# Kernel tuning notes

Measured on AMD Instinct MI355X. Metric: run time of the kernel, lower is better.

The kernel has to match this reference:

```python
import jax, jax.numpy as jnp
import numpy as np

C = 64  # chunk size, fixed in the original module


def setup_inputs() -> dict:
    key = jax.random.key(0)
    k1, k2, k3, k4, k5 = jax.random.split(key, 5)
    B, T, D, H = 4, 4096, 1024, 8
    out = jax.random.normal(k1, (B, T, D), jnp.float32)
    W_write = jax.random.normal(k2, (D, D), jnp.float32) * 0.02
    # original inits proj_read to zeros; use small random weight so the memory path is exercised
    W_read = jax.random.normal(k3, (D, D), jnp.float32) * 0.02
    W_beta = jax.random.normal(k4, (H, D), jnp.float32) * 0.02
    decay = 4.6 + jax.random.normal(k5, (H,), jnp.float32) * 0.1
    return {"out": out, "W_write": W_write, "W_read": W_read, "W_beta": W_beta, "decay": decay}


def reference(out, W_write, W_read, W_beta, decay):
    B, T, D = out.shape
    H = decay.shape[0]
    d = D // H
    assert T % C == 0  # chosen shapes avoid padding (pad_len == 0 path)
    N = T // C

    x = out.astype(jnp.float32)
    xh = x.reshape(B, T, H, d)
    rk = xh / jnp.maximum(jnp.linalg.norm(xh, axis=-1, keepdims=True), 1e-12)
    rk = rk.transpose(0, 2, 1, 3)                                   # (B,H,T,d) read keys
    wk = jnp.pad(rk[:, :, :-1], ((0, 0), (0, 0), (1, 0), (0, 0)))    # write keys = shifted read keys
    v = (x @ W_write.T).reshape(B, T, H, d).transpose(0, 2, 1, 3)    # (B,H,T,d)
    beta = jax.nn.sigmoid(x @ W_beta.T).transpose(0, 2, 1)[..., None]  # (B,H,T,1)
    v = v * beta
    wk_beta = wk * beta

    log_gamma = jnp.log(jax.nn.sigmoid(decay))                       # (H,)
    pos = jnp.arange(C, dtype=jnp.float32)
    cum_decay = (pos + 1.0) * log_gamma[:, None]                     # (H,C)
    tril = jnp.tril(jnp.ones((C, C), jnp.float32))
    L_mask = jnp.exp((cum_decay[:, :, None] - cum_decay[:, None, :]) * tril) * tril  # (H,C,C)
    decay_exp = jnp.exp(cum_decay)[:, :, None]                       # (H,C,1)
    chunk_total = jnp.exp(cum_decay[:, -1])[:, None, None]           # (H,1,1)
    dw = jnp.exp(cum_decay[:, -1:] - cum_decay)[:, :, None]          # (H,C,1)

    rk_c = rk.reshape(B, H, N, C, d)
    wk_c = wk.reshape(B, H, N, C, d)
    v_c = v.reshape(B, H, N, C, d)
    wkb_c = wk_beta.reshape(B, H, N, C, d)

    # UT transform: A = strictly-lower part of -(beta K)(K^T) with decay, then forward substitution
    strict_lower = jnp.tril(jnp.ones((C, C), bool), -1)
    A = -(wkb_c @ jnp.swapaxes(wk_c, -1, -2)) * L_mask[None, :, None]
    A = jnp.where(strict_lower, A, 0.0)

    def ut_body(i, A):
        row = A[..., i, :]                                           # (B,H,N,C)
        new_row = row + jnp.einsum('bhnj,bhnjk->bhnk', row, A)
        return A.at[..., i, :].set(new_row)

    A = jax.lax.fori_loop(1, C, ut_body, A)
    A = A + jnp.eye(C, dtype=A.dtype)

    v_c = A @ v_c
    wk_cum = A @ (wkb_c * decay_exp[None, :, None])

    # cross-chunk state recurrence
    causal = jnp.tril(jnp.ones((C, C), bool))                        # keep diag + lower
    xs = (jnp.moveaxis(rk_c, 2, 0), jnp.moveaxis(wk_c, 2, 0),
          jnp.moveaxis(v_c, 2, 0), jnp.moveaxis(wk_cum, 2, 0))
    S0 = jnp.zeros((B, H, d, d), jnp.float32)

    def chunk_step(S, xs_i):
        rk_i, wk_i, v_i, wkc_i = xs_i                                # each (B,H,C,d)
        attn = (rk_i @ jnp.swapaxes(wk_i, -1, -2)) * L_mask[None]
        attn = jnp.where(causal, attn, 0.0)
        v_new = v_i - wkc_i @ S
        o_i = (rk_i * decay_exp[None]) @ S + attn @ v_new
        S_new = chunk_total[None] * S + jnp.swapaxes(wk_i * dw[None], -1, -2) @ v_new
        return S_new, o_i

    _, o = jax.lax.scan(chunk_step, S0, xs)                          # (N,B,H,C,d)
    o = jnp.moveaxis(o, 0, 2).reshape(B, H, T, d).transpose(0, 2, 1, 3).reshape(B, T, D)
    return out + (o @ W_read.T).astype(out.dtype)
```

## Files before the change

kernel.cpp:

```cpp
#include <hip/hip_runtime.h>
#include <hip/hip_bf16.h>
#include <math.h>


#define T_LEN 4096
typedef unsigned short ushort;
typedef __attribute__((ext_vector_type(2))) unsigned short us2;
typedef __attribute__((ext_vector_type(4))) unsigned short us4;
typedef __attribute__((ext_vector_type(8))) unsigned short us8;
typedef __attribute__((ext_vector_type(8))) short short8v;
typedef __attribute__((ext_vector_type(4))) float f32x4;

__device__ __forceinline__ float bf2f(ushort u) {
  union { unsigned int u; float f; } c; c.u = ((unsigned int)u) << 16; return c.f;
}
__device__ __forceinline__ ushort f2bf(float x) {
  union { float f; unsigned int u; } c; c.f = x;
  unsigned int u = c.u + 0x7FFFu + ((c.u >> 16) & 1u);
  return (ushort)(u >> 16);
}

__global__ __launch_bounds__(256) void k_wcvt(
    const float* __restrict__ Ww, const float* __restrict__ Wr,
    ushort* __restrict__ Wwb, ushort* __restrict__ Wrb)
{
  size_t i = ((size_t)blockIdx.x * 256 + threadIdx.x) * 8;
  float4 p0 = *(const float4*)(Ww + i), p1 = *(const float4*)(Ww + i + 4);
  us8 o;
  o[0]=f2bf(p0.x); o[1]=f2bf(p0.y); o[2]=f2bf(p0.z); o[3]=f2bf(p0.w);
  o[4]=f2bf(p1.x); o[5]=f2bf(p1.y); o[6]=f2bf(p1.z); o[7]=f2bf(p1.w);
  *(us8*)(Wwb + i) = o;
  float4 q0 = *(const float4*)(Wr + i), q1 = *(const float4*)(Wr + i + 4);
  us8 o2;
  o2[0]=f2bf(q0.x); o2[1]=f2bf(q0.y); o2[2]=f2bf(q0.z); o2[3]=f2bf(q0.w);
  o2[4]=f2bf(q1.x); o2[5]=f2bf(q1.y); o2[6]=f2bf(q1.z); o2[7]=f2bf(q1.w);
  *(us8*)(Wrb + i) = o2;
}

__global__ __launch_bounds__(128) void k_prep(
    const float* __restrict__ x, const float* __restrict__ Wb,
    ushort* __restrict__ rk, float* __restrict__ beta, ushort* __restrict__ xb)
{
  int bt = blockIdx.x;
  int b = bt >> 12, t = bt & 4095;
  int tid = threadIdx.x;
  __shared__ float xs[1024];
  __shared__ float red[16];
  {
    const float4* x4 = (const float4*)(x + (size_t)bt * 1024);
    float4* xs4 = (float4*)xs;
    xs4[tid] = x4[tid];
    xs4[tid + 128] = x4[tid + 128];
  }
  __syncthreads();
  int h = tid >> 4;
  int e0 = h * 128 + (tid & 15) * 8;
  float ss = 0.f;
  #pragma unroll
  for (int s = 0; s < 8; ++s) { float v = xs[e0 + s]; ss += v * v; }
  #pragma unroll
  for (int m = 1; m < 16; m <<= 1) ss += __shfl_xor(ss, m, 64);
  float inv = 1.f / fmaxf(sqrtf(ss), 1e-12f);
  {
    int bh = b * 8 + h;
    us8 o;
    #pragma unroll
    for (int s = 0; s < 8; ++s) o[s] = f2bf(xs[e0 + s] * inv);
    *(us8*)(rk + ((size_t)bh * T_LEN + t) * 128 + (tid & 15) * 8) = o;
  }
  {
    us8 o;
    #pragma unroll
    for (int s = 0; s < 8; ++s) o[s] = f2bf(xs[tid * 8 + s]);
    *(us8*)(xb + (size_t)bt * 1024 + tid * 8) = o;
  }
  const float* xk = xs + tid * 8;
  #pragma unroll
  for (int h2 = 0; h2 < 8; ++h2) {
    const float* wb = Wb + (size_t)h2 * 1024 + tid * 8;
    float p = 0.f;
    #pragma unroll
    for (int s = 0; s < 8; ++s) p += xk[s] * wb[s];
    #pragma unroll
    for (int m = 1; m < 64; m <<= 1) p += __shfl_xor(p, m, 64);
    if ((tid & 63) == 0) red[(tid >> 6) * 8 + h2] = p;
  }
  __syncthreads();
  if (tid < 8) {
    float s = red[tid] + red[8 + tid];
    beta[((size_t)(b * 8 + tid)) * T_LEN + t] = 1.f / (1.f + expf(-s));
  }
}

#define LDK 40
template<int MODE>
__global__ __launch_bounds__(256) void k_gemm(
    const ushort* __restrict__ A, const ushort* __restrict__ Wb,
    const float* __restrict__ beta, const float* __restrict__ xadd,
    void* __restrict__ out_)
{
  __shared__ ushort As[128 * LDK];
  __shared__ ushort Bs[128 * LDK];
  const int n0 = blockIdx.x * 128;
  const int m0 = blockIdx.y * 128;
  const int tid = threadIdx.x;
  const int lane = tid & 63;
  const int wid = tid >> 6;
  const int wr = wid >> 1, wc = wid & 1;
  const int c = lane & 15, g = lane >> 4;
  const int srow = tid >> 2;
  const int seg = tid & 3;

  f32x4 acc[4][4] = {};

  for (int k0 = 0; k0 < 1024; k0 += 32) {
    {
      us8 o0 = *(const us8*)(A + (size_t)(m0 + srow) * 1024 + k0 + seg * 8);
      us8 o1 = *(const us8*)(A + (size_t)(m0 + srow + 64) * 1024 + k0 + seg * 8);
      *(us8*)&As[srow * LDK + seg * 8] = o0;
      *(us8*)&As[(srow + 64) * LDK + seg * 8] = o1;
    }
    {
      us8 o0 = *(const us8*)(Wb + (size_t)(n0 + srow) * 1024 + k0 + seg * 8);
      us8 o1 = *(const us8*)(Wb + (size_t)(n0 + srow + 64) * 1024 + k0 + seg * 8);
      *(us8*)&Bs[srow * LDK + seg * 8] = o0;
      *(us8*)&Bs[(srow + 64) * LDK + seg * 8] = o1;
    }
    __syncthreads();
    short8v af[4], bf[4];
    #pragma unroll
    for (int mi = 0; mi < 4; ++mi)
      af[mi] = *(const short8v*)&As[(wr * 64 + mi * 16 + c) * LDK + g * 8];
    #pragma unroll
    for (int ni = 0; ni < 4; ++ni)
      bf[ni] = *(const short8v*)&Bs[(wc * 64 + ni * 16 + c) * LDK + g * 8];
    #pragma unroll
    for (int mi = 0; mi < 4; ++mi)
      #pragma unroll
      for (int ni = 0; ni < 4; ++ni)
        acc[mi][ni] = __builtin_amdgcn_mfma_f32_16x16x32_bf16(af[mi], bf[ni], acc[mi][ni], 0, 0, 0);
    __syncthreads();
  }

  if (MODE == 0) {
    ushort* vb = (ushort*)out_;
    const int hh = n0 >> 7;
    #pragma unroll
    for (int mi = 0; mi < 4; ++mi) {
      #pragma unroll
      for (int ni = 0; ni < 4; ++ni) {
        int jc = wc * 64 + ni * 16 + c;
        #pragma unroll
        for (int j = 0; j < 4; ++j) {
          int m = m0 + wr * 64 + mi * 16 + g * 4 + j;
          int b = m >> 12, t = m & 4095;
          size_t base = (size_t)(b * 8 + hh) * T_LEN + t;
          float bv = beta[base];
          vb[base * 128 + jc] = f2bf(acc[mi][ni][j] * bv);
        }
      }
    }
  } else {
    float* out = (float*)out_;
    #pragma unroll
    for (int mi = 0; mi < 4; ++mi) {
      #pragma unroll
      for (int ni = 0; ni < 4; ++ni) {
        int n = n0 + wc * 64 + ni * 16 + c;
        #pragma unroll
        for (int j = 0; j < 4; ++j) {
          int m = m0 + wr * 64 + mi * 16 + g * 4 + j;
          size_t idx = (size_t)m * 1024 + n;
          out[idx] = xadd[idx] + acc[mi][ni][j];
        }
      }
    }
  }
}

__global__ __launch_bounds__(256) void k_chunk(
    const ushort* __restrict__ rk, ushort* __restrict__ vb,
    ushort* __restrict__ wkcum, ushort* __restrict__ attn,
    const float* __restrict__ beta, const float* __restrict__ decay,
    ushort* __restrict__ wkdwT)
{
  int bh = blockIdx.x >> 6;
  int n = blockIdx.x & 63;
  int h = bh & 7;
  int tid = threadIdx.x;
  int lane = tid & 63, w = tid >> 6;
  int c = lane & 15, g = lane >> 4;

  __shared__ __align__(16) char smem[39952];
  ushort* rkb  = (ushort*)smem;
  float*  redp = (float*)smem;
  ushort* Ab1  = (ushort*)smem;
  ushort* Ab2  = (ushort*)(smem + 9216);
  float*  Af   = (float*)(smem + 21760);
  ushort* xT   = (ushort*)(smem + 18432);
  float*  gpow  = (float*)(smem + 39168);
  float*  betaS = (float*)(smem + 39432);
  float*  bd    = (float*)(smem + 39688);

  float lg = logf(1.f / (1.f + expf(-decay[h])));
  if (tid < 65) gpow[tid] = expf(lg * (float)tid);
  if (tid < 64) betaS[tid] = beta[(size_t)bh * T_LEN + n * 64 + tid];
  const int t0 = n * 64;
  const size_t bhbase = (size_t)bh * T_LEN;
  const us8 zero8 = {0, 0, 0, 0, 0, 0, 0, 0};

  #pragma unroll
  for (int u = 0; u < 5; ++u) {
    int idx = tid + u * 256;
    int row = idx >> 4, cb = idx & 15;
    us8 v = zero8;
    int t = t0 + row - 1;
    if (row <= 64 && t >= 0) v = *(const us8*)(rk + (bhbase + t) * 128 + cb * 8);
    *(us8*)&rkb[row * 136 + cb * 8] = v;
  }
  for (int idx = tid; idx < 64 * 68; idx += 256) Af[idx] = 0.f;
  __syncthreads();
  if (tid < 64) bd[tid] = betaS[tid] * gpow[tid + 1];

  const size_t abase = ((size_t)bh * 64 + n) * 4096;
  {
    const int TR[14] = {0,1,1,2,2,2,3,3,3,3,4,4,4,4};
    const int TC[14] = {0,0,1,0,1,2,0,1,2,3,0,1,2,3};
    #pragma unroll
    for (int ti = 0; ti < 14; ++ti) {
      if ((ti & 3) != w) continue;
      const int tr = TR[ti], tc = TC[ti];
      f32x4 acc = {0.f, 0.f, 0.f, 0.f};
      #pragma unroll
      for (int ks = 0; ks < 4; ++ks) {
        short8v a = *(const short8v*)&rkb[(tr * 16 + c) * 136 + ks * 32 + g * 8];
        short8v b = *(const short8v*)&rkb[(tc * 16 + c) * 136 + ks * 32 + g * 8];
        acc = __builtin_amdgcn_mfma_f32_16x16x32_bf16(a, b, acc, 0, 0, 0);
      }
      #pragma unroll
      for (int r = 0; r < 4; ++r) {
        int a_ = tr * 16 + g * 4 + r;
        int j = tc * 16 + c;
        float val = acc[r];
        if (a_ <= 63) Af[a_ * 68 + j] = (a_ > j) ? (-betaS[a_] * val * gpow[a_ - j]) : 0.f;
        if (a_ >= 1 && a_ <= 64) {
          if (j <= a_ - 1)      attn[abase + (size_t)(a_ - 1) * 64 + j] = f2bf(val * gpow[a_ - 1 - j]);
          else if (a_ <= 63)    attn[abase + (size_t)(a_ - 1) * 64 + j] = 0;
        }
      }
    }
  }
  {
    const int ZR[6] = {0,0,0,1,1,2};
    const int ZC[6] = {1,2,3,2,3,3};
    int rr = tid >> 4, cc2 = tid & 15;
    #pragma unroll
    for (int z = 0; z < 6; ++z) {
      int r_att = ZR[z] * 16 - 1 + rr;
      if (r_att >= 0) attn[abase + (size_t)r_att * 64 + ZC[z] * 16 + cc2] = 0;
    }
  }
  __syncthreads();

  {
    int k = tid & 63, sp = tid >> 6;
    for (int i = 1; i < 64; ++i) {
      float part = 0.f;
      #pragma unroll
      for (int jj = 0; jj < 16; ++jj) {
        int j = sp * 16 + jj;
        part += Af[i * 68 + j] * Af[j * 68 + k];
      }
      redp[sp * 64 + k] = part;
      __syncthreads();
      if (tid < 64) Af[i * 68 + tid] += redp[tid] + redp[64 + tid] + redp[128 + tid] + redp[192 + tid];
      __syncthreads();
    }
  }
  {
    int i = tid >> 2, j0 = (tid & 3) * 16;
    #pragma unroll
    for (int jj = 0; jj < 16; ++jj) {
      int j = j0 + jj;
      float av = Af[i * 68 + j] + ((i == j) ? 1.f : 0.f);
      Ab1[i * 72 + j] = f2bf(av * bd[j]);
      Ab2[i * 72 + j] = f2bf(av);
    }
  }
  __syncthreads();

  #pragma unroll
  for (int u = 0; u < 4; ++u) {
    int idx = tid + u * 256;
    int j = idx & 63, eb = idx >> 6;
    int t = t0 + j - 1;
    us8 v = zero8;
    if (t >= 0) v = *(const us8*)(rk + (bhbase + t) * 128 + eb * 8);
    #pragma unroll
    for (int s = 0; s < 8; ++s) xT[(eb * 8 + s) * 72 + j] = v[s];
  }
  __syncthreads();

  {
    f32x4 acc[8] = {};
    #pragma unroll
    for (int ks = 0; ks < 2; ++ks) {
      short8v a = *(const short8v*)&Ab1[(w * 16 + c) * 72 + ks * 32 + g * 8];
      #pragma unroll
      for (int nt = 0; nt < 8; ++nt) {
        short8v b = *(const short8v*)&xT[(nt * 16 + c) * 72 + ks * 32 + g * 8];
        acc[nt] = __builtin_amdgcn_mfma_f32_16x16x32_bf16(a, b, acc[nt], 0, 0, 0);
      }
    }
    #pragma unroll
    for (int nt = 0; nt < 8; ++nt)
      #pragma unroll
      for (int r = 0; r < 4; ++r) {
        int i = w * 16 + g * 4 + r, e = nt * 16 + c;
        wkcum[(bhbase + t0 + i) * 128 + e] = f2bf(acc[nt][r]);
      }
  }
  {
    const size_t kbase = ((size_t)bh * 64 + n) * 8192;
    #pragma unroll
    for (int u = 0; u < 4; ++u) {
      int idx = tid + u * 256;
      int e = idx >> 3, seg = idx & 7;
      us8 v = *(const us8*)&xT[e * 72 + seg * 8];
      us8 o;
      #pragma unroll
      for (int s = 0; s < 8; ++s) o[s] = f2bf(bf2f(v[s]) * gpow[63 - (seg * 8 + s)]);
      *(us8*)(wkdwT + kbase + (size_t)e * 64 + seg * 8) = o;
    }
  }
  __syncthreads();
  #pragma unroll
  for (int u = 0; u < 4; ++u) {
    int idx = tid + u * 256;
    int j = idx & 63, eb = idx >> 6;
    us8 v = *(const us8*)(vb + (bhbase + t0 + j) * 128 + eb * 8);
    #pragma unroll
    for (int s = 0; s < 8; ++s) xT[(eb * 8 + s) * 72 + j] = v[s];
  }
  __syncthreads();
  {
    f32x4 acc[8] = {};
    #pragma unroll
    for (int ks = 0; ks < 2; ++ks) {
      short8v a = *(const short8v*)&Ab2[(w * 16 + c) * 72 + ks * 32 + g * 8];
      #pragma unroll
      for (int nt = 0; nt < 8; ++nt) {
        short8v b = *(const short8v*)&xT[(nt * 16 + c) * 72 + ks * 32 + g * 8];
        acc[nt] = __builtin_amdgcn_mfma_f32_16x16x32_bf16(a, b, acc[nt], 0, 0, 0);
      }
    }
    #pragma unroll
    for (int nt = 0; nt < 8; ++nt)
      #pragma unroll
      for (int r = 0; r < 4; ++r) {
        int i = w * 16 + g * 4 + r, e = nt * 16 + c;
        vb[(bhbase + t0 + i) * 128 + e] = f2bf(acc[nt][r]);
      }
  }
}

#define SCAN_STEP(W_, R_, T_, K_, V_, nW, nR, nT, nK, nV, n_) {                 \
  const int t0s = (n_) * 64;                                                    \
  { const int np = ((n_) < 63) ? (n_) + 1 : 63;                                 \
    const size_t rb = (bhbase + (size_t)(np * 64 + 16 * w + c)) * 128;          \
    _Pragma("unroll")                                                           \
    for (int ks = 0; ks < 4; ++ks) {                                            \
      nW[ks] = *(const short8v*)(wkcum + rb + ks * 32 + g * 8);                 \
      nR[ks] = *(const short8v*)(rk    + rb + ks * 32 + g * 8); }               \
    const size_t ab = ((size_t)bh * 64 + np) * 4096 + (size_t)(16 * w + c) * 64;\
    nT[0] = *(const short8v*)(attn + ab + g * 8);                               \
    nT[1] = *(const short8v*)(attn + ab + 32 + g * 8);                          \
    const size_t kb = ((size_t)bh * 64 + np) * 8192;                            \
    nK[0] = *(const short8v*)(wkdwT + kb + (size_t)(32 * w + c) * 64 + g * 8);  \
    nK[1] = *(const short8v*)(wkdwT + kb + (size_t)(32 * w + c) * 64 + 32 + g * 8); \
    nK[2] = *(const short8v*)(wkdwT + kb + (size_t)(32 * w + 16 + c) * 64 + g * 8); \
    nK[3] = *(const short8v*)(wkdwT + kb + (size_t)(32 * w + 16 + c) * 64 + 32 + g * 8); \
    _Pragma("unroll")                                                           \
    for (int r = 0; r < 4; ++r)                                                 \
      nV[r] = vb[(bhbase + (size_t)(np * 64 + 16 * w + 4 * g + r)) * 128 + q0 + c]; } \
  f32x4 accA = {}, accB = {};                                                   \
  _Pragma("unroll")                                                             \
  for (int ks = 0; ks < 4; ++ks) {                                              \
    short8v b0 = *(const short8v*)&ST[c * 136 + ks * 32 + g * 8];               \
    accA = __builtin_amdgcn_mfma_f32_16x16x32_bf16(W_[ks], b0, accA, 0, 0, 0);  \
    accB = __builtin_amdgcn_mfma_f32_16x16x32_bf16(R_[ks], b0, accB, 0, 0, 0); }\
  _Pragma("unroll")                                                             \
  for (int r = 0; r < 4; ++r) {                                                 \
    int i = 16 * w + 4 * g + r;                                                 \
    accB[r] *= gB[r];                                                           \
    vnL[c * 72 + i] = f2bf(bf2f(V_[r]) - accA[r]); }                            \
  asm volatile("s_waitcnt lgkmcnt(0)" ::: "memory");                            \
  __builtin_amdgcn_s_barrier();                                                 \
  short8v vf0 = *(const short8v*)&vnL[c * 72 + g * 8];                          \
  short8v vf1 = *(const short8v*)&vnL[c * 72 + 32 + g * 8];                     \
  accB = __builtin_amdgcn_mfma_f32_16x16x32_bf16(T_[0], vf0, accB, 0, 0, 0);    \
  accB = __builtin_amdgcn_mfma_f32_16x16x32_bf16(T_[1], vf1, accB, 0, 0, 0);    \
  _Pragma("unroll")                                                             \
  for (int r = 0; r < 4; ++r) {                                                 \
    int i = 16 * w + 4 * g + r;                                                 \
    og[((size_t)b_ * T_LEN + t0s + i) * 1024 + h * 128 + q0 + c] = f2bf(accB[r]); } \
  _Pragma("unroll")                                                             \
  for (int r = 0; r < 4; ++r) { accS0[r] *= ct; accS1[r] *= ct; }               \
  accS0 = __builtin_amdgcn_mfma_f32_16x16x32_bf16(K_[0], vf0, accS0, 0, 0, 0);  \
  accS0 = __builtin_amdgcn_mfma_f32_16x16x32_bf16(K_[1], vf1, accS0, 0, 0, 0);  \
  accS1 = __builtin_amdgcn_mfma_f32_16x16x32_bf16(K_[2], vf0, accS1, 0, 0, 0);  \
  accS1 = __builtin_amdgcn_mfma_f32_16x16x32_bf16(K_[3], vf1, accS1, 0, 0, 0);  \
  _Pragma("unroll")                                                             \
  for (int r = 0; r < 4; ++r) {                                                 \
    int p0r = 32 * w + 4 * g + r;                                               \
    ST[c * 136 + p0r]      = f2bf(accS0[r]);                                    \
    ST[c * 136 + p0r + 16] = f2bf(accS1[r]); }                                  \
  asm volatile("s_waitcnt lgkmcnt(0)" ::: "memory");                            \
  __builtin_amdgcn_s_barrier();                                                 \
}

__global__ __launch_bounds__(256) void k_scan_fused(
    const ushort* __restrict__ rk, const ushort* __restrict__ vb,
    const ushort* __restrict__ wkcum, const ushort* __restrict__ attn,
    const ushort* __restrict__ wkdwT, const float* __restrict__ decay,
    ushort* __restrict__ og)
{
  const int bh = blockIdx.x & 31;
  const int q0 = (blockIdx.x >> 5) * 16;
  const int b_ = bh >> 3, h = bh & 7;
  const int tid = threadIdx.x;
  const int lane = tid & 63, w = tid >> 6;
  const int c = lane & 15, g = lane >> 4;

  __shared__ ushort ST[16 * 136];
  __shared__ ushort vnL[16 * 72];
  __shared__ float gpow[65];

  float lg = logf(1.f / (1.f + expf(-decay[h])));
  if (tid < 65) gpow[tid] = expf(lg * (float)tid);
  for (int idx = tid; idx < 16 * 136; idx += 256) ST[idx] = 0;
  __syncthreads();
  const float ct = gpow[64];
  float gB[4];
  #pragma unroll
  for (int r = 0; r < 4; ++r) gB[r] = gpow[16 * w + 4 * g + r + 1];
  const size_t bhbase = (size_t)bh * T_LEN;

  f32x4 accS0 = {}, accS1 = {};
  short8v aW[4], aR[4], aT[2], aK[4];
  short8v bW[4], bR[4], bT[2], bK[4];
  ushort aV[4], bV[4];
  {
    const size_t rb = (bhbase + (size_t)(16 * w + c)) * 128;
    #pragma unroll
    for (int ks = 0; ks < 4; ++ks) {
      aW[ks] = *(const short8v*)(wkcum + rb + ks * 32 + g * 8);
      aR[ks] = *(const short8v*)(rk + rb + ks * 32 + g * 8);
    }
    const size_t ab = (size_t)bh * 64 * 4096 + (size_t)(16 * w + c) * 64;
    aT[0] = *(const short8v*)(attn + ab + g * 8);
    aT[1] = *(const short8v*)(attn + ab + 32 + g * 8);
    const size_t kb = (size_t)bh * 64 * 8192;
    aK[0] = *(const short8v*)(wkdwT + kb + (size_t)(32 * w + c) * 64 + g * 8);
    aK[1] = *(const short8v*)(wkdwT + kb + (size_t)(32 * w + c) * 64 + 32 + g * 8);
    aK[2] = *(const short8v*)(wkdwT + kb + (size_t)(32 * w + 16 + c) * 64 + g * 8);
    aK[3] = *(const short8v*)(wkdwT + kb + (size_t)(32 * w + 16 + c) * 64 + 32 + g * 8);
    #pragma unroll
    for (int r = 0; r < 4; ++r)
      aV[r] = vb[(bhbase + (size_t)(16 * w + 4 * g + r)) * 128 + q0 + c];
  }
  for (int n = 0; n < 64; n += 2) {
    SCAN_STEP(aW, aR, aT, aK, aV, bW, bR, bT, bK, bV, n);
    SCAN_STEP(bW, bR, bT, bK, bV, aW, aR, aT, aK, aV, n + 1);
  }
}

extern "C" void kernel_launch(void* const* d_in, const int* in_sizes, int n_in,
                              void* d_out, int out_size, void* d_ws, size_t ws_size,
                              hipStream_t stream) {
  const float* x   = (const float*)d_in[0];
  const float* Ww  = (const float*)d_in[1];
  const float* Wr  = (const float*)d_in[2];
  const float* Wb  = (const float*)d_in[3];
  const float* dec = (const float*)d_in[4];
  float* out = (float*)d_out;
  ushort* ws = (ushort*)d_ws;
  const size_t SZ = 16777216ull;
  ushort* rk    = ws;
  ushort* vb    = ws + SZ;
  ushort* wkcum = ws + 2 * SZ;
  ushort* og    = ws + 3 * SZ;
  ushort* attn  = ws + 4 * SZ;
  float*  beta  = (float*)(ws + 4 * SZ + 8388608ull);
  ushort* wkdwT = ws + 4 * SZ + 8388608ull + 262144ull;
  ushort* Wwb   = ws + 92536832ull;
  ushort* Wrb   = ws + 93585408ull;
  ushort* xb    = og;
  const size_t NEED = 189267968ull;
  if (ws_size < NEED) {
    hipMemcpyAsync(d_out, (const void*)x, (size_t)out_size * 4, hipMemcpyDeviceToDevice, stream);
    return;
  }

  k_wcvt<<<dim3(512), dim3(256), 0, stream>>>(Ww, Wr, Wwb, Wrb);
  k_prep<<<dim3(16384), dim3(128), 0, stream>>>(x, Wb, rk, beta, xb);
  k_gemm<0><<<dim3(8, 128), dim3(256), 0, stream>>>(xb, Wwb, beta, nullptr, (void*)vb);
  k_chunk<<<dim3(2048), dim3(256), 0, stream>>>(rk, vb, wkcum, attn, beta, dec, wkdwT);
  k_scan_fused<<<dim3(256), dim3(256), 0, stream>>>(rk, vb, wkcum, attn, wkdwT, dec, og);
  k_gemm<1><<<dim3(8, 128), dim3(256), 0, stream>>>(og, Wrb, nullptr, (const float*)x, (void*)out);
}
```

Measured before the change: 384.7 us.

## Run scan with a single wavefront per block to remove barriers

```diff
diff --git a/kernel.cpp b/kernel.cpp
--- a/kernel.cpp
+++ b/kernel.cpp
@@ -364,62 +364,103 @@
   }
 }
 
-#define SCAN_STEP(W_, R_, T_, K_, V_, nW, nR, nT, nK, nV, n_) {                 \
+#define SCAN1(CURW, CURV, NXTW, NXTV, n_) {                                     \
   const int t0s = (n_) * 64;                                                    \
+                                               \
   { const int np = ((n_) < 63) ? (n_) + 1 : 63;                                 \
-    const size_t rb = (bhbase + (size_t)(np * 64 + 16 * w + c)) * 128;          \
-    _Pragma("unroll")                                                           \
-    for (int ks = 0; ks < 4; ++ks) {                                            \
-      nW[ks] = *(const short8v*)(wkcum + rb + ks * 32 + g * 8);                 \
-      nR[ks] = *(const short8v*)(rk    + rb + ks * 32 + g * 8); }               \
-    const size_t ab = ((size_t)bh * 64 + np) * 4096 + (size_t)(16 * w + c) * 64;\
-    nT[0] = *(const short8v*)(attn + ab + g * 8);                               \
-    nT[1] = *(const short8v*)(attn + ab + 32 + g * 8);                          \
-    const size_t kb = ((size_t)bh * 64 + np) * 8192;                            \
-    nK[0] = *(const short8v*)(wkdwT + kb + (size_t)(32 * w + c) * 64 + g * 8);  \
-    nK[1] = *(const short8v*)(wkdwT + kb + (size_t)(32 * w + c) * 64 + 32 + g * 8); \
-    nK[2] = *(const short8v*)(wkdwT + kb + (size_t)(32 * w + 16 + c) * 64 + g * 8); \
-    nK[3] = *(const short8v*)(wkdwT + kb + (size_t)(32 * w + 16 + c) * 64 + 32 + g * 8); \
-    _Pragma("unroll")                                                           \
-    for (int r = 0; r < 4; ++r)                                                 \
-      nV[r] = vb[(bhbase + (size_t)(np * 64 + 16 * w + 4 * g + r)) * 128 + q0 + c]; } \
-  f32x4 accA = {}, accB = {};                                                   \
-  _Pragma("unroll")                                                             \
-  for (int ks = 0; ks < 4; ++ks) {                                              \
-    short8v b0 = *(const short8v*)&ST[c * 136 + ks * 32 + g * 8];               \
-    accA = __builtin_amdgcn_mfma_f32_16x16x32_bf16(W_[ks], b0, accA, 0, 0, 0);  \
-    accB = __builtin_amdgcn_mfma_f32_16x16x32_bf16(R_[ks], b0, accB, 0, 0, 0); }\
-  _Pragma("unroll")                                                             \
-  for (int r = 0; r < 4; ++r) {                                                 \
-    int i = 16 * w + 4 * g + r;                                                 \
-    accB[r] *= gB[r];                                                           \
-    vnL[c * 72 + i] = f2bf(bf2f(V_[r]) - accA[r]); }                            \
-  asm volatile("s_waitcnt lgkmcnt(0)" ::: "memory");                            \
-  __builtin_amdgcn_s_barrier();                                                 \
-  short8v vf0 = *(const short8v*)&vnL[c * 72 + g * 8];                          \
-  short8v vf1 = *(const short8v*)&vnL[c * 72 + 32 + g * 8];                     \
-  accB = __builtin_amdgcn_mfma_f32_16x16x32_bf16(T_[0], vf0, accB, 0, 0, 0);    \
-  accB = __builtin_amdgcn_mfma_f32_16x16x32_bf16(T_[1], vf1, accB, 0, 0, 0);    \
-  _Pragma("unroll")                                                             \
-  for (int r = 0; r < 4; ++r) {                                                 \
-    int i = 16 * w + 4 * g + r;                                                 \
-    og[((size_t)b_ * T_LEN + t0s + i) * 1024 + h * 128 + q0 + c] = f2bf(accB[r]); } \
-  _Pragma("unroll")                                                             \
-  for (int r = 0; r < 4; ++r) { accS0[r] *= ct; accS1[r] *= ct; }               \
-  accS0 = __builtin_amdgcn_mfma_f32_16x16x32_bf16(K_[0], vf0, accS0, 0, 0, 0);  \
-  accS0 = __builtin_amdgcn_mfma_f32_16x16x32_bf16(K_[1], vf1, accS0, 0, 0, 0);  \
-  accS1 = __builtin_amdgcn_mfma_f32_16x16x32_bf16(K_[2], vf0, accS1, 0, 0, 0);  \
-  accS1 = __builtin_amdgcn_mfma_f32_16x16x32_bf16(K_[3], vf1, accS1, 0, 0, 0);  \
-  _Pragma("unroll")                                                             \
-  for (int r = 0; r < 4; ++r) {                                                 \
-    int p0r = 32 * w + 4 * g + r;                                               \
-    ST[c * 136 + p0r]      = f2bf(accS0[r]);                                    \
-    ST[c * 136 + p0r + 16] = f2bf(accS1[r]); }                                  \
-  asm volatile("s_waitcnt lgkmcnt(0)" ::: "memory");                            \
-  __builtin_amdgcn_s_barrier();                                                 \
-}
-
-__global__ __launch_bounds__(256) void k_scan_fused(
+    _Pragma("unroll")                                                           \
+    for (int ti = 0; ti < 4; ++ti) {                                            \
+      const size_t rb = (bhbase + (size_t)(np * 64 + 16 * ti + c)) * 128;       \
+      _Pragma("unroll")                                                         \
+      for (int ks = 0; ks < 4; ++ks)                                            \
+        NXTW[ti][ks] = *(const short8v*)(wkcum + rb + ks * 32 + g * 8);         \
+      _Pragma("unroll")                                                         \
+      for (int r = 0; r < 4; ++r)                                               \
+        NXTV[ti][r] = vb[(bhbase + (size_t)(np * 64 + 16 * ti + 4 * g + r)) * 128 + q0 + c]; \
+    } }                                                                         \
+                                               \
+  short8v aR[4][4], aT[4][2], aK[8][2];                                         \
+  const size_t ab = ((size_t)bh * 64 + (n_)) * 4096;                            \
+  const size_t kb = ((size_t)bh * 64 + (n_)) * 8192;                            \
+  _Pragma("unroll")                                                             \
+  for (int ti = 0; ti < 4; ++ti) {                                              \
+    const size_t rb = (bhbase + (size_t)(t0s + 16 * ti + c)) * 128;             \
+    _Pragma("unroll")                                                           \
+    for (int ks = 0; ks < 4; ++ks)                                              \
+      aR[ti][ks] = *(const short8v*)(rk + rb + ks * 32 + g * 8);                \
+    _Pragma("unroll")                                                           \
+    for (int kv = 0; kv < 2; ++kv)                                              \
+      aT[ti][kv] = *(const short8v*)(attn + ab + (size_t)(16 * ti + c) * 64 + kv * 32 + g * 8); \
+  }                                                                             \
+                                \
+  short8v stb[4];                                                               \
+  _Pragma("unroll")                                                             \
+  for (int ks = 0; ks < 4; ++ks)                                                \
+    stb[ks] = *(const short8v*)&ST[c * 136 + ks * 32 + g * 8];                  \
+                                                          \
+  f32x4 accA[4] = {};                                                           \
+  _Pragma("unroll")                                                             \
+  for (int ti = 0; ti < 4; ++ti)                                                \
+    _Pragma("unroll")                                                           \
+    for (int ks = 0; ks < 4; ++ks)                                              \
+      accA[ti] = __builtin_amdgcn_mfma_f32_16x16x32_bf16(CURW[ti][ks], stb[ks], accA[ti], 0, 0, 0); \
+                                                    \
+  _Pragma("unroll")                                                             \
+  for (int ti = 0; ti < 4; ++ti) {                                              \
+    us4 o;                                                                      \
+    _Pragma("unroll")                                                           \
+    for (int r = 0; r < 4; ++r) o[r] = f2bf(bf2f(CURV[ti][r]) - accA[ti][r]);   \
+    *(us4*)&vnL[c * 72 + 16 * ti + 4 * g] = o;                                  \
+  }                                                                             \
+                                                      \
+  _Pragma("unroll")                                                             \
+  for (int pt = 0; pt < 8; ++pt)                                                \
+    _Pragma("unroll")                                                           \
+    for (int kv = 0; kv < 2; ++kv)                                              \
+      aK[pt][kv] = *(const short8v*)(wkdwT + kb + (size_t)(16 * pt + c) * 64 + kv * 32 + g * 8); \
+                                                     \
+  f32x4 accB[4] = {};                                                           \
+  _Pragma("unroll")                                                             \
+  for (int ti = 0; ti < 4; ++ti) {                                              \
+    _Pragma("unroll")                                                           \
+    for (int ks = 0; ks < 4; ++ks)                                              \
+      accB[ti] = __builtin_amdgcn_mfma_f32_16x16x32_bf16(aR[ti][ks], stb[ks], accB[ti], 0, 0, 0); \
+    _Pragma("unroll")                                                           \
+    for (int r = 0; r < 4; ++r) accB[ti][r] *= gB[ti][r];                       \
+  }                                                                             \
+                                 \
+  short8v vnb[2];                                                               \
+  _Pragma("unroll")                                                             \
+  for (int kv = 0; kv < 2; ++kv)                                                \
+    vnb[kv] = *(const short8v*)&vnL[c * 72 + kv * 32 + g * 8];                  \
+                                            \
+  _Pragma("unroll")                                                             \
+  for (int ti = 0; ti < 4; ++ti) {                                              \
+    _Pragma("unroll")                                                           \
+    for (int kv = 0; kv < 2; ++kv)                                              \
+      accB[ti] = __builtin_amdgcn_mfma_f32_16x16x32_bf16(aT[ti][kv], vnb[kv], accB[ti], 0, 0, 0); \
+    _Pragma("unroll")                                                           \
+    for (int r = 0; r < 4; ++r) {                                               \
+      int i = 16 * ti + 4 * g + r;                                              \
+      og[((size_t)b_ * T_LEN + t0s + i) * 1024 + h * 128 + q0 + c] = f2bf(accB[ti][r]); \
+    }                                                                           \
+  }                                                                             \
+                                   \
+  _Pragma("unroll")                                                             \
+  for (int pt = 0; pt < 8; ++pt) {                                              \
+    _Pragma("unroll")                                                           \
+    for (int r = 0; r < 4; ++r) accS[pt][r] *= ct;                              \
+    _Pragma("unroll")                                                           \
+    for (int kv = 0; kv < 2; ++kv)                                              \
+      accS[pt] = __builtin_amdgcn_mfma_f32_16x16x32_bf16(aK[pt][kv], vnb[kv], accS[pt], 0, 0, 0); \
+    us4 o;                                                                      \
+    _Pragma("unroll")                                                           \
+    for (int r = 0; r < 4; ++r) o[r] = f2bf(accS[pt][r]);                       \
+    *(us4*)&ST[c * 136 + 16 * pt + 4 * g] = o;                                  \
+  }                                                                             \
+}
+
+__global__ __launch_bounds__(64, 1) void k_scan_fused(
     const ushort* __restrict__ rk, const ushort* __restrict__ vb,
     const ushort* __restrict__ wkcum, const ushort* __restrict__ attn,
     const ushort* __restrict__ wkdwT, const float* __restrict__ decay,
@@ -428,50 +469,39 @@
   const int bh = blockIdx.x & 31;
   const int q0 = (blockIdx.x >> 5) * 16;
   const int b_ = bh >> 3, h = bh & 7;
-  const int tid = threadIdx.x;
-  const int lane = tid & 63, w = tid >> 6;
+  const int lane = threadIdx.x;
   const int c = lane & 15, g = lane >> 4;
 
   __shared__ ushort ST[16 * 136];
   __shared__ ushort vnL[16 * 72];
-  __shared__ float gpow[65];
 
   float lg = logf(1.f / (1.f + expf(-decay[h])));
-  if (tid < 65) gpow[tid] = expf(lg * (float)tid);
-  for (int idx = tid; idx < 16 * 136; idx += 256) ST[idx] = 0;
-  __syncthreads();
-  const float ct = gpow[64];
-  float gB[4];
-  #pragma unroll
-  for (int r = 0; r < 4; ++r) gB[r] = gpow[16 * w + 4 * g + r + 1];
+  float gB[4][4];
+  #pragma unroll
+  for (int ti = 0; ti < 4; ++ti)
+    #pragma unroll
+    for (int r = 0; r < 4; ++r)
+      gB[ti][r] = expf(lg * (float)(16 * ti + 4 * g + r + 1));
+  const float ct = expf(lg * 64.f);
+  for (int idx = lane; idx < 16 * 136; idx += 64) ST[idx] = 0;
   const size_t bhbase = (size_t)bh * T_LEN;
 
-  f32x4 accS0 = {}, accS1 = {};
-  short8v aW[4], aR[4], aT[2], aK[4];
-  short8v bW[4], bR[4], bT[2], bK[4];
-  ushort aV[4], bV[4];
-  {
-    const size_t rb = (bhbase + (size_t)(16 * w + c)) * 128;
-    #pragma unroll
-    for (int ks = 0; ks < 4; ++ks) {
-      aW[ks] = *(const short8v*)(wkcum + rb + ks * 32 + g * 8);
-      aR[ks] = *(const short8v*)(rk + rb + ks * 32 + g * 8);
-    }
-    const size_t ab = (size_t)bh * 64 * 4096 + (size_t)(16 * w + c) * 64;
-    aT[0] = *(const short8v*)(attn + ab + g * 8);
-    aT[1] = *(const short8v*)(attn + ab + 32 + g * 8);
-    const size_t kb = (size_t)bh * 64 * 8192;
-    aK[0] = *(const short8v*)(wkdwT + kb + (size_t)(32 * w + c) * 64 + g * 8);
-    aK[1] = *(const short8v*)(wkdwT + kb + (size_t)(32 * w + c) * 64 + 32 + g * 8);
-    aK[2] = *(const short8v*)(wkdwT + kb + (size_t)(32 * w + 16 + c) * 64 + g * 8);
-    aK[3] = *(const short8v*)(wkdwT + kb + (size_t)(32 * w + 16 + c) * 64 + 32 + g * 8);
+  f32x4 accS[8] = {};
+  short8v aWa[4][4], aWb[4][4];
+  ushort  vVa[4][4], vVb[4][4];
+  #pragma unroll
+  for (int ti = 0; ti < 4; ++ti) {
+    const size_t rb = (bhbase + (size_t)(16 * ti + c)) * 128;
+    #pragma unroll
+    for (int ks = 0; ks < 4; ++ks)
+      aWa[ti][ks] = *(const short8v*)(wkcum + rb + ks * 32 + g * 8);
     #pragma unroll
     for (int r = 0; r < 4; ++r)
-      aV[r] = vb[(bhbase + (size_t)(16 * w + 4 * g + r)) * 128 + q0 + c];
+      vVa[ti][r] = vb[(bhbase + (size_t)(16 * ti + 4 * g + r)) * 128 + q0 + c];
   }
   for (int n = 0; n < 64; n += 2) {
-    SCAN_STEP(aW, aR, aT, aK, aV, bW, bR, bT, bK, bV, n);
-    SCAN_STEP(bW, bR, bT, bK, bV, aW, aR, aT, aK, aV, n + 1);
+    SCAN1(aWa, vVa, aWb, vVb, n);
+    SCAN1(aWb, vVb, aWa, vVa, n + 1);
   }
 }
 
@@ -506,6 +536,6 @@
   k_prep<<<dim3(16384), dim3(128), 0, stream>>>(x, Wb, rk, beta, xb);
   k_gemm<0><<<dim3(8, 128), dim3(256), 0, stream>>>(xb, Wwb, beta, nullptr, (void*)vb);
   k_chunk<<<dim3(2048), dim3(256), 0, stream>>>(rk, vb, wkcum, attn, beta, dec, wkdwT);
-  k_scan_fused<<<dim3(256), dim3(256), 0, stream>>>(rk, vb, wkcum, attn, wkdwT, dec, og);
+  k_scan_fused<<<dim3(256), dim3(64), 0, stream>>>(rk, vb, wkcum, attn, wkdwT, dec, og);
   k_gemm<1><<<dim3(8, 128), dim3(256), 0, stream>>>(og, Wrb, nullptr, (const float*)x, (void*)out);
 }
```

New measurement: 727.4 us. +89.1%, slower.
